# Kernel tuning notes

Hardware: AMD Instinct MI355X
Metric: run time of the kernel (lower is better)

The kernel has to match this reference:

```python
import jax, jax.numpy as jnp
import numpy as np

B, D = 65536, 365

def _linp(k, fan_in, fan_out):
    # torch nn.Linear default init: U(-1/sqrt(fan_in), 1/sqrt(fan_in))
    kw, kb = jax.random.split(k)
    bound = 1.0 / np.sqrt(fan_in)
    W = jax.random.uniform(kw, (fan_in, fan_out), jnp.float32, -bound, bound)
    b = jax.random.uniform(kb, (fan_out,), jnp.float32, -bound, bound)
    return W, b

def setup_inputs() -> dict:
    key = jax.random.key(0)
    ks = jax.random.split(key, 9)
    x = jax.random.normal(ks[0], (B, D), jnp.float32)
    W1, b1 = _linp(ks[1], D, 512)
    W2, b2 = _linp(ks[2], 512, 256)
    W3, b3 = _linp(ks[3], 256, 128)
    Ws, bs = _linp(ks[4], 6, 32)
    Wc1, bc1 = _linp(ks[5], 128 + 32, 64)
    Wc2, bc2 = _linp(ks[6], 64, 32)
    Wc3, bc3 = _linp(ks[7], 32, 1)
    return dict(x=x, W1=W1, b1=b1, W2=W2, b2=b2, W3=W3, b3=b3,
                Ws=Ws, bs=bs, Wc1=Wc1, bc1=bc1, Wc2=Wc2, bc2=bc2,
                Wc3=Wc3, bc3=bc3)

def _row_stats(x):
    # fused row-wise moments: mean, std (ddof=1), min, max, skew, kurtosis
    mu = jnp.mean(x, axis=1, keepdims=True)          # [B,1]
    c = x - mu                                        # [B,D]
    var1 = jnp.sum(c * c, axis=1) / (x.shape[1] - 1)  # unbiased, matches torch.std()
    sigma = jnp.sqrt(var1)
    m3 = jnp.mean(c ** 3, axis=1)
    m4 = jnp.mean(c ** 4, axis=1)
    skew = m3 / (sigma ** 3 + 1e-8)
    kurt = m4 / (sigma ** 4 + 1e-8)
    return jnp.stack([mu[:, 0], sigma, jnp.min(x, axis=1), jnp.max(x, axis=1), skew, kurt], axis=1)

def reference(x, W1, b1, W2, b2, W3, b3, Ws, bs, Wc1, bc1, Wc2, bc2, Wc3, bc3):
    h = jax.nn.relu(x @ W1 + b1)
    h = jax.nn.relu(h @ W2 + b2)
    seq = jax.nn.relu(h @ W3 + b3)            # [B,128]
    stat = _row_stats(x) @ Ws + bs            # [B,32]
    comb = jnp.concatenate([seq, stat], axis=1)
    c = jax.nn.relu(comb @ Wc1 + bc1)
    c = jax.nn.relu(c @ Wc2 + bc2)
    out = jax.nn.sigmoid(c @ Wc3 + bc3)       # [B,1]
    return out[:, 0]
```

## Files before the change

### kernel.cpp

```cpp
#include <hip/hip_runtime.h>
#include <math.h>

typedef __attribute__((ext_vector_type(8)))  short short8;
typedef __attribute__((ext_vector_type(16))) float float16;

#define DEVI __device__ __forceinline__

DEVI short f2bf(float f) {
    unsigned u = __float_as_uint(f);
    u = (u + 0x7fffu + ((u >> 16) & 1u)) >> 16;
    return (short)u;
}
DEVI unsigned pk2(float a, float b) {
    return (unsigned)(unsigned short)f2bf(a) | ((unsigned)(unsigned short)f2bf(b) << 16);
}
DEVI float16 mfma16(short8 a, short8 b, float16 c) {
    return __builtin_amdgcn_mfma_f32_32x32x16_bf16(a, b, c, 0, 0, 0);
}
DEVI int rowof(int r, int h) { return (r & 3) + 8 * (r >> 2) + 4 * h; }
DEVI short8 lds8(const short* p) { return *(const short8*)p; }
DEVI short8 gld8(const short* p) { return *(const short8*)p; }

#define W1T_OFF  0
#define W2T_OFF  188416
#define W3T_OFF  319488
#define WC1T_OFF 352256
#define WC2T_OFF 362496

__global__ void prep_v2(const float* __restrict__ W1, const float* __restrict__ W2,
                        const float* __restrict__ W3, const float* __restrict__ Wc1,
                        const float* __restrict__ Wc2, short* __restrict__ ws) {
    __shared__ short T[16 * 72];
    int b = blockIdx.x, t = threadIdx.x;
    const float* src; int K, N; size_t base; int kc, nb;
    if (b < 184)        {            src = W1;  K = 365; N = 512; base = W1T_OFF;  kc = b >> 3;  nb = b & 7; }
    else if (b < 312)   { int l = b - 184; src = W2;  K = 512; N = 256; base = W2T_OFF;  kc = l >> 2;  nb = l & 3; }
    else if (b < 344)   { int l = b - 312; src = W3;  K = 256; N = 128; base = W3T_OFF;  kc = l >> 1;  nb = l & 1; }
    else if (b < 354)   {            src = Wc1; K = 160; N = 64;  base = WC1T_OFF; kc = b - 344; nb = 0; }
    else                {            src = Wc2; K = 64;  N = 32;  base = WC2T_OFF; kc = b - 354; nb = 0; }
    int n = nb * 64 + (t & 63);
    int kr = t >> 6;
    #pragma unroll
    for (int i = 0; i < 4; ++i) {
        int krow = kr + 4 * i;
        int k = kc * 16 + krow;
        float v = (k < K && n < N) ? src[(size_t)k * N + n] : 0.f;
        T[krow * 72 + (t & 63)] = f2bf(v);
    }
    __syncthreads();
    int n2 = t >> 2, ksq = (t & 3) * 4;
    int ng = nb * 64 + n2;
    if (ng < N) {
        unsigned lo = (unsigned)(unsigned short)T[ksq * 72 + n2]
                    | ((unsigned)(unsigned short)T[(ksq + 1) * 72 + n2] << 16);
        unsigned hi = (unsigned)(unsigned short)T[(ksq + 2) * 72 + n2]
                    | ((unsigned)(unsigned short)T[(ksq + 3) * 72 + n2] << 16);
        uint2 d; d.x = lo; d.y = hi;
        *(uint2*)(ws + base + ((size_t)kc * N + ng) * 16 + ksq) = d;
    }
}

__global__ __launch_bounds__(512, 4)
void fused_v4(const float* __restrict__ x,
              const float* __restrict__ b1f, const float* __restrict__ b2f,
              const float* __restrict__ b3f, const float* __restrict__ Wsf,
              const float* __restrict__ bsf, const float* __restrict__ bc1f,
              const float* __restrict__ bc2f, const float* __restrict__ Wc3f,
              const float* __restrict__ bc3f,
              const short* __restrict__ wsw, float* __restrict__ out)
{
    __shared__ __align__(16) char smem[65536];
    short* XT    = (short*)smem;
    short* SB    = (short*)(smem + 48128);
    short* C1    = (short*)smem;
    short* FEATL = (short*)(smem + 12288);
    float* C2    = (float*)(smem + 20480);

    const short* W1t  = wsw + W1T_OFF;
    const short* W2t  = wsw + W2T_OFF;
    const short* W3t  = wsw + W3T_OFF;
    const short* Wc1t = wsw + WC1T_OFF;
    const short* Wc2t = wsw + WC2T_OFF;

    const int tid  = (int)threadIdx.x;
    const int lane = tid & 63;
    const int wv   = tid >> 6;
    const int m    = lane & 31;
    const int h    = lane >> 5;
    const int rowBase = (int)blockIdx.x * 64;

    float bb1a = b1f[32 * wv + m];
    float bb1b = b1f[256 + 32 * wv + m];
    float bb2  = b2f[32 * wv + m];
    float bb3  = b3f[32 * (wv & 3) + m];

    const int r0 = tid >> 3, j0 = tid & 7;
    const float* xrow = x + (size_t)(rowBase + r0) * 365;
    float s1 = 0.f, s2 = 0.f, s3 = 0.f, s4 = 0.f, mn = 1e30f, mx = -1e30f;
    #pragma unroll
    for (int i = 0; i < 6; ++i) {
        int o = j0 + 8 * i;
        if (o <= 45) {
            float xf[8];
            #pragma unroll
            for (int jj = 0; jj < 8; ++jj) {
                int col = o * 8 + jj;
                xf[jj] = (col < 365) ? xrow[col] : 0.f;
            }
            #pragma unroll
            for (int jj = 0; jj < 8; ++jj) {
                int col = o * 8 + jj;
                if (col < 365) {
                    float v = xf[jj], v2 = v * v;
                    s1 += v; s2 += v2; s3 += v2 * v; s4 += v2 * v2;
                    mn = fminf(mn, v); mx = fmaxf(mx, v);
                }
            }
            int4 w4;
            w4.x = (int)pk2(xf[0], xf[1]); w4.y = (int)pk2(xf[2], xf[3]);
            w4.z = (int)pk2(xf[4], xf[5]); w4.w = (int)pk2(xf[6], xf[7]);
            *(int4*)(XT + r0 * 376 + o * 8) = w4;
        }
    }
    #pragma unroll
    for (int off = 1; off <= 4; off <<= 1) {
        s1 += __shfl_xor(s1, off); s2 += __shfl_xor(s2, off);
        s3 += __shfl_xor(s3, off); s4 += __shfl_xor(s4, off);
        mn = fminf(mn, __shfl_xor(mn, off)); mx = fmaxf(mx, __shfl_xor(mx, off));
    }
    unsigned fdw0, fdw1;
    {
        float mean  = s1 * (1.0f / 365.0f);
        float var1  = (s2 - 365.0f * mean * mean) * (1.0f / 364.0f);
        float sigma = sqrtf(var1);
        float m3 = (s3 - 3.0f * mean * s2) * (1.0f / 365.0f) + 2.0f * mean * mean * mean;
        float mm = mean * mean;
        float m4 = (s4 - 4.0f * mean * s3 + 6.0f * mm * s2) * (1.0f / 365.0f) - 3.0f * mm * mm;
        float sg2 = sigma * sigma;
        float skew = m3 / (sigma * sg2 + 1e-8f);
        float kurt = m4 / (sg2 * sg2 + 1e-8f);
        float st[6] = { mean, sigma, mn, mx, skew, kurt };
        float f[4];
        #pragma unroll
        for (int c0 = 0; c0 < 4; ++c0) {
            int c = 4 * j0 + c0;
            float acc = bsf[c];
            #pragma unroll
            for (int jj = 0; jj < 6; ++jj) acc += st[jj] * Wsf[jj * 32 + c];
            f[c0] = acc;
        }
        fdw0 = pk2(f[0], f[1]); fdw1 = pk2(f[2], f[3]);
    }
    __syncthreads();

    float16 ha0, ha1;
    #pragma unroll
    for (int i = 0; i < 16; ++i) { ha0[i] = 0.f; ha1[i] = 0.f; }

    const short* Ap0  = XT + m * 376 + h * 8;
    const short* Ap1  = XT + (32 + m) * 376 + h * 8;
    const short* A2p0 = SB + m * 136 + h * 8;
    const short* A2p1 = SB + (32 + m) * 136 + h * 8;
    const int stcol = 32 * (wv & 3) + m;

    #pragma unroll
    for (int p = 0; p < 2; ++p) {
        float16 ga0, ga1;
        #pragma unroll
        for (int i = 0; i < 16; ++i) { ga0[i] = 0.f; ga1[i] = 0.f; }
        const short* B1 = W1t + (256 * p + 32 * wv + m) * 16 + h * 8;
        #pragma unroll
        for (int kc = 0; kc < 23; ++kc) {
            short8 b  = gld8(B1 + kc * 8192);
            short8 a0 = lds8(Ap0 + kc * 16);
            short8 a1 = lds8(Ap1 + kc * 16);
            ga0 = mfma16(a0, b, ga0);
            ga1 = mfma16(a1, b, ga1);
        }
        float bb = p ? bb1b : bb1a;
        #pragma unroll
        for (int s = 0; s < 2; ++s) {
            int sl = 2 * p + s;
            __syncthreads();
            if ((wv >> 2) == s) {
                #pragma unroll
                for (int r = 0; r < 16; ++r) {
                    SB[rowof(r, h) * 136 + stcol]        = f2bf(fmaxf(ga0[r] + bb, 0.f));
                    SB[(32 + rowof(r, h)) * 136 + stcol] = f2bf(fmaxf(ga1[r] + bb, 0.f));
                }
            }
            __syncthreads();
            const short* B2 = W2t + sl * 8 * 4096 + (32 * wv + m) * 16 + h * 8;
            #pragma unroll
            for (int i = 0; i < 8; ++i) {
                short8 b  = gld8(B2 + i * 4096);
                short8 a0 = lds8(A2p0 + i * 16);
                short8 a1 = lds8(A2p1 + i * 16);
                ha0 = mfma16(a0, b, ha0);
                ha1 = mfma16(a1, b, ha1);
            }
        }
    }

    float16 g3;
    #pragma unroll
    for (int i = 0; i < 16; ++i) g3[i] = 0.f;
    const short* A3p = SB + ((wv >> 2) * 32 + m) * 136 + h * 8;
    #pragma unroll
    for (int t = 0; t < 2; ++t) {
        __syncthreads();
        if ((wv >> 2) == t) {
            #pragma unroll
            for (int r = 0; r < 16; ++r) {
                SB[rowof(r, h) * 136 + stcol]        = f2bf(fmaxf(ha0[r] + bb2, 0.f));
                SB[(32 + rowof(r, h)) * 136 + stcol] = f2bf(fmaxf(ha1[r] + bb2, 0.f));
            }
        }
        __syncthreads();
        const short* B3 = W3t + t * 8 * 2048 + (32 * (wv & 3) + m) * 16 + h * 8;
        #pragma unroll
        for (int i = 0; i < 8; ++i) {
            short8 b = gld8(B3 + i * 2048);
            short8 a = lds8(A3p + i * 16);
            g3 = mfma16(a, b, g3);
        }
    }

    __syncthreads();
    {
        int rb = (wv >> 2) * 32;
        #pragma unroll
        for (int r = 0; r < 16; ++r)
            SB[(rb + rowof(r, h)) * 136 + stcol] = f2bf(fmaxf(g3[r] + bb3, 0.f));
        *(unsigned*)(FEATL + r0 * 40 + 4 * j0)     = fdw0;
        *(unsigned*)(FEATL + r0 * 40 + 4 * j0 + 2) = fdw1;
    }
    __syncthreads();

    if (wv < 4) {
        int m4 = wv & 1, c4 = wv >> 1;
        const short* B4 = Wc1t + (32 * c4 + m) * 16 + h * 8;
        const short* A4 = SB + (m4 * 32 + m) * 136 + h * 8;
        float16 g4;
        #pragma unroll
        for (int i = 0; i < 16; ++i) g4[i] = 0.f;
        #pragma unroll
        for (int i = 0; i < 8; ++i) {
            short8 b = gld8(B4 + i * 1024);
            short8 a = lds8(A4 + i * 16);
            g4 = mfma16(a, b, g4);
        }
        const short* AF = FEATL + (m4 * 32 + m) * 40 + h * 8;
        #pragma unroll
        for (int i = 0; i < 2; ++i) {
            short8 b = gld8(B4 + (8 + i) * 1024);
            short8 a = lds8(AF + i * 16);
            g4 = mfma16(a, b, g4);
        }
        float bb = bc1f[32 * c4 + m];
        #pragma unroll
        for (int r = 0; r < 16; ++r)
            C1[(m4 * 32 + rowof(r, h)) * 72 + 32 * c4 + m] = f2bf(fmaxf(g4[r] + bb, 0.f));
    }
    __syncthreads();

    if (wv < 2) {
        const short* B5 = Wc2t + m * 16 + h * 8;
        const short* A5 = C1 + (wv * 32 + m) * 72 + h * 8;
        float16 g5;
        #pragma unroll
        for (int i = 0; i < 16; ++i) g5[i] = 0.f;
        #pragma unroll
        for (int i = 0; i < 4; ++i) {
            short8 b = gld8(B5 + i * 512);
            short8 a = lds8(A5 + i * 16);
            g5 = mfma16(a, b, g5);
        }
        float bb = bc2f[m];
        #pragma unroll
        for (int r = 0; r < 16; ++r)
            C2[(wv * 32 + rowof(r, h)) * 33 + m] = fmaxf(g5[r] + bb, 0.f);
    }
    __syncthreads();

    if (tid < 64) {
        float z = bc3f[0];
        #pragma unroll
        for (int i = 0; i < 32; ++i) z += C2[tid * 33 + i] * Wc3f[i];
        out[rowBase + tid] = 1.0f / (1.0f + expf(-z));
    }
}

extern "C" void kernel_launch(void* const* d_in, const int* in_sizes, int n_in,
                              void* d_out, int out_size, void* d_ws, size_t ws_size,
                              hipStream_t stream)
{
    (void)in_sizes; (void)n_in; (void)out_size; (void)ws_size;
    const float* x   = (const float*)d_in[0];
    const float* W1  = (const float*)d_in[1];
    const float* b1  = (const float*)d_in[2];
    const float* W2  = (const float*)d_in[3];
    const float* b2  = (const float*)d_in[4];
    const float* W3  = (const float*)d_in[5];
    const float* b3  = (const float*)d_in[6];
    const float* Ws  = (const float*)d_in[7];
    const float* bs  = (const float*)d_in[8];
    const float* Wc1 = (const float*)d_in[9];
    const float* bc1 = (const float*)d_in[10];
    const float* Wc2 = (const float*)d_in[11];
    const float* bc2 = (const float*)d_in[12];
    const float* Wc3 = (const float*)d_in[13];
    const float* bc3 = (const float*)d_in[14];
    short* ws = (short*)d_ws;

    prep_v2<<<358, 256, 0, stream>>>(W1, W2, W3, Wc1, Wc2, ws);
    fused_v4<<<1024, 512, 0, stream>>>(x, b1, b2, b3, Ws, bs, bc1, bc2, Wc3, bc3,
                                       ws, (float*)d_out);
}
```

Before: 236.6 us.

## Halve block to 4 waves with 2x2 MFMA tiles and double-buffered LDS stages

The fused MLP kernel moves from 8 to 4 waves per 64-row block. Each wave now computes two column tiles by two row tiles, so every global weight fragment feeds twice as many MFMAs. Layer-1 outputs are held in registers as packed bf16 and written to two alternating LDS staging buffers, which removes many barriers. Register pressure rises a lot (four float16 accumulators plus the packed layer-1 array), and with fewer waves per CU there is less latency hiding.

```diff
diff --git a/kernel.cpp b/kernel.cpp
--- a/kernel.cpp
+++ b/kernel.cpp
@@ -60,8 +60,8 @@
     }
 }
 
-__global__ __launch_bounds__(512, 4)
-void fused_v4(const float* __restrict__ x,
+__global__ __launch_bounds__(256, 2)
+void fused_v5(const float* __restrict__ x,
               const float* __restrict__ b1f, const float* __restrict__ b2f,
               const float* __restrict__ b3f, const float* __restrict__ Wsf,
               const float* __restrict__ bsf, const float* __restrict__ bc1f,
@@ -69,12 +69,12 @@
               const float* __restrict__ bc3f,
               const short* __restrict__ wsw, float* __restrict__ out)
 {
-    __shared__ __align__(16) char smem[65536];
+    __shared__ __align__(16) char smem[53248];
     short* XT    = (short*)smem;
-    short* SB    = (short*)(smem + 48128);
-    short* C1    = (short*)smem;
-    short* FEATL = (short*)(smem + 12288);
-    float* C2    = (float*)(smem + 20480);
+    short* SB0   = (short*)smem;
+    short* SB1   = (short*)(smem + 17408);
+    float* C2f   = (float*)(smem + 36864);
+    short* FEATL = (short*)(smem + 48128);
 
     const short* W1t  = wsw + W1T_OFF;
     const short* W2t  = wsw + W2T_OFF;
@@ -89,17 +89,23 @@
     const int h    = lane >> 5;
     const int rowBase = (int)blockIdx.x * 64;
 
-    float bb1a = b1f[32 * wv + m];
-    float bb1b = b1f[256 + 32 * wv + m];
-    float bb2  = b2f[32 * wv + m];
-    float bb3  = b3f[32 * (wv & 3) + m];
-
-    const int r0 = tid >> 3, j0 = tid & 7;
+    float bb1[2][2], bb2[2];
+    #pragma unroll
+    for (int p = 0; p < 2; ++p)
+    #pragma unroll
+    for (int ct = 0; ct < 2; ++ct) bb1[p][ct] = b1f[256 * p + 64 * wv + 32 * ct + m];
+    bb2[0] = b2f[64 * wv + m]; bb2[1] = b2f[64 * wv + 32 + m];
+    float bb3  = b3f[32 * wv + m];
+    float bbc1 = bc1f[32 * (wv & 1) + m];
+    float bbc2 = bc2f[m];
+
+    const int r0 = tid >> 2, q = tid & 2 ? (tid & 3) : (tid & 3);
+    const int qq = tid & 3;
     const float* xrow = x + (size_t)(rowBase + r0) * 365;
     float s1 = 0.f, s2 = 0.f, s3 = 0.f, s4 = 0.f, mn = 1e30f, mx = -1e30f;
     #pragma unroll
-    for (int i = 0; i < 6; ++i) {
-        int o = j0 + 8 * i;
+    for (int i = 0; i < 12; ++i) {
+        int o = qq + 4 * i;
         if (o <= 45) {
             float xf[8];
             #pragma unroll
@@ -123,12 +129,11 @@
         }
     }
     #pragma unroll
-    for (int off = 1; off <= 4; off <<= 1) {
+    for (int off = 1; off <= 2; off <<= 1) {
         s1 += __shfl_xor(s1, off); s2 += __shfl_xor(s2, off);
         s3 += __shfl_xor(s3, off); s4 += __shfl_xor(s4, off);
         mn = fminf(mn, __shfl_xor(mn, off)); mx = fmaxf(mx, __shfl_xor(mx, off));
     }
-    unsigned fdw0, fdw1;
     {
         float mean  = s1 * (1.0f / 365.0f);
         float var1  = (s2 - 365.0f * mean * mean) * (1.0f / 364.0f);
@@ -140,153 +145,180 @@
         float skew = m3 / (sigma * sg2 + 1e-8f);
         float kurt = m4 / (sg2 * sg2 + 1e-8f);
         float st[6] = { mean, sigma, mn, mx, skew, kurt };
-        float f[4];
-        #pragma unroll
-        for (int c0 = 0; c0 < 4; ++c0) {
-            int c = 4 * j0 + c0;
+        float f[8];
+        #pragma unroll
+        for (int c0 = 0; c0 < 8; ++c0) {
+            int c = 8 * qq + c0;
             float acc = bsf[c];
             #pragma unroll
             for (int jj = 0; jj < 6; ++jj) acc += st[jj] * Wsf[jj * 32 + c];
             f[c0] = acc;
         }
-        fdw0 = pk2(f[0], f[1]); fdw1 = pk2(f[2], f[3]);
-    }
-    __syncthreads();
-
-    float16 ha0, ha1;
-    #pragma unroll
-    for (int i = 0; i < 16; ++i) { ha0[i] = 0.f; ha1[i] = 0.f; }
-
-    const short* Ap0  = XT + m * 376 + h * 8;
-    const short* Ap1  = XT + (32 + m) * 376 + h * 8;
-    const short* A2p0 = SB + m * 136 + h * 8;
-    const short* A2p1 = SB + (32 + m) * 136 + h * 8;
-    const int stcol = 32 * (wv & 3) + m;
-
+        int4 w4;
+        w4.x = (int)pk2(f[0], f[1]); w4.y = (int)pk2(f[2], f[3]);
+        w4.z = (int)pk2(f[4], f[5]); w4.w = (int)pk2(f[6], f[7]);
+        *(int4*)(FEATL + r0 * 40 + 8 * qq) = w4;
+    }
+    __syncthreads();
+
+    const short* Ap0 = XT + m * 376 + h * 8;
+    const short* Ap1 = Ap0 + 32 * 376;
+    unsigned park[2][2][2][8];
     #pragma unroll
     for (int p = 0; p < 2; ++p) {
-        float16 ga0, ga1;
-        #pragma unroll
-        for (int i = 0; i < 16; ++i) { ga0[i] = 0.f; ga1[i] = 0.f; }
-        const short* B1 = W1t + (256 * p + 32 * wv + m) * 16 + h * 8;
+        float16 c00, c01, c10, c11;
+        #pragma unroll
+        for (int i = 0; i < 16; ++i) { c00[i] = 0.f; c01[i] = 0.f; c10[i] = 0.f; c11[i] = 0.f; }
+        const short* B1 = W1t + (256 * p + 64 * wv + m) * 16 + h * 8;
         #pragma unroll
         for (int kc = 0; kc < 23; ++kc) {
-            short8 b  = gld8(B1 + kc * 8192);
+            short8 b0 = gld8(B1 + kc * 8192);
+            short8 b1 = gld8(B1 + 512 + kc * 8192);
             short8 a0 = lds8(Ap0 + kc * 16);
             short8 a1 = lds8(Ap1 + kc * 16);
-            ga0 = mfma16(a0, b, ga0);
-            ga1 = mfma16(a1, b, ga1);
-        }
-        float bb = p ? bb1b : bb1a;
-        #pragma unroll
-        for (int s = 0; s < 2; ++s) {
-            int sl = 2 * p + s;
-            __syncthreads();
-            if ((wv >> 2) == s) {
-                #pragma unroll
-                for (int r = 0; r < 16; ++r) {
-                    SB[rowof(r, h) * 136 + stcol]        = f2bf(fmaxf(ga0[r] + bb, 0.f));
-                    SB[(32 + rowof(r, h)) * 136 + stcol] = f2bf(fmaxf(ga1[r] + bb, 0.f));
-                }
+            c00 = mfma16(a0, b0, c00);
+            c01 = mfma16(a1, b0, c01);
+            c10 = mfma16(a0, b1, c10);
+            c11 = mfma16(a1, b1, c11);
+        }
+        #pragma unroll
+        for (int rr = 0; rr < 8; ++rr) {
+            park[p][0][0][rr] = pk2(fmaxf(c00[2*rr] + bb1[p][0], 0.f), fmaxf(c00[2*rr+1] + bb1[p][0], 0.f));
+            park[p][0][1][rr] = pk2(fmaxf(c01[2*rr] + bb1[p][0], 0.f), fmaxf(c01[2*rr+1] + bb1[p][0], 0.f));
+            park[p][1][0][rr] = pk2(fmaxf(c10[2*rr] + bb1[p][1], 0.f), fmaxf(c10[2*rr+1] + bb1[p][1], 0.f));
+            park[p][1][1][rr] = pk2(fmaxf(c11[2*rr] + bb1[p][1], 0.f), fmaxf(c11[2*rr+1] + bb1[p][1], 0.f));
+        }
+    }
+    __syncthreads();
+
+    float16 H00, H01, H10, H11;
+    #pragma unroll
+    for (int i = 0; i < 16; ++i) { H00[i] = 0.f; H01[i] = 0.f; H10[i] = 0.f; H11[i] = 0.f; }
+    const short* A2r0 = SB0 + m * 136 + h * 8;
+    #pragma unroll
+    for (int s = 0; s < 4; ++s) {
+        short* SBs = (s & 1) ? SB1 : SB0;
+        if ((wv >> 1) == (s & 1)) {
+            int p = s >> 1;
+            int cb = 64 * (wv & 1) + m;
+            #pragma unroll
+            for (int ct = 0; ct < 2; ++ct)
+            #pragma unroll
+            for (int rt = 0; rt < 2; ++rt)
+            #pragma unroll
+            for (int rr = 0; rr < 8; ++rr) {
+                unsigned pv = park[p][ct][rt][rr];
+                int row = rt * 32 + rowof(2 * rr, h);
+                SBs[row * 136 + cb + 32 * ct]       = (short)(pv & 0xffffu);
+                SBs[(row + 1) * 136 + cb + 32 * ct] = (short)(pv >> 16);
             }
-            __syncthreads();
-            const short* B2 = W2t + sl * 8 * 4096 + (32 * wv + m) * 16 + h * 8;
-            #pragma unroll
-            for (int i = 0; i < 8; ++i) {
-                short8 b  = gld8(B2 + i * 4096);
-                short8 a0 = lds8(A2p0 + i * 16);
-                short8 a1 = lds8(A2p1 + i * 16);
-                ha0 = mfma16(a0, b, ha0);
-                ha1 = mfma16(a1, b, ha1);
+        }
+        __syncthreads();
+        const short* A0p = SBs + m * 136 + h * 8;
+        const short* A1p = A0p + 32 * 136;
+        const short* B2 = W2t + (64 * wv + m) * 16 + h * 8 + s * 32768;
+        #pragma unroll
+        for (int i = 0; i < 8; ++i) {
+            short8 b0 = gld8(B2 + i * 4096);
+            short8 b1 = gld8(B2 + 512 + i * 4096);
+            short8 a0 = lds8(A0p + i * 16);
+            short8 a1 = lds8(A1p + i * 16);
+            H00 = mfma16(a0, b0, H00);
+            H01 = mfma16(a1, b0, H01);
+            H10 = mfma16(a0, b1, H10);
+            H11 = mfma16(a1, b1, H11);
+        }
+    }
+    (void)A2r0;
+
+    float16 S0, S1;
+    #pragma unroll
+    for (int i = 0; i < 16; ++i) { S0[i] = 0.f; S1[i] = 0.f; }
+    #pragma unroll
+    for (int t = 0; t < 2; ++t) {
+        short* SBs = t ? SB1 : SB0;
+        if ((wv >> 1) == t) {
+            int cb = 64 * (wv & 1) + m;
+            #pragma unroll
+            for (int rr = 0; rr < 8; ++rr) {
+                int rw0 = rowof(2 * rr, h);
+                SBs[rw0 * 136 + cb]              = f2bf(fmaxf(H00[2*rr]   + bb2[0], 0.f));
+                SBs[(rw0 + 1) * 136 + cb]        = f2bf(fmaxf(H00[2*rr+1] + bb2[0], 0.f));
+                SBs[(32 + rw0) * 136 + cb]       = f2bf(fmaxf(H01[2*rr]   + bb2[0], 0.f));
+                SBs[(33 + rw0) * 136 + cb]       = f2bf(fmaxf(H01[2*rr+1] + bb2[0], 0.f));
+                SBs[rw0 * 136 + cb + 32]         = f2bf(fmaxf(H10[2*rr]   + bb2[1], 0.f));
+                SBs[(rw0 + 1) * 136 + cb + 32]   = f2bf(fmaxf(H10[2*rr+1] + bb2[1], 0.f));
+                SBs[(32 + rw0) * 136 + cb + 32]  = f2bf(fmaxf(H11[2*rr]   + bb2[1], 0.f));
+                SBs[(33 + rw0) * 136 + cb + 32]  = f2bf(fmaxf(H11[2*rr+1] + bb2[1], 0.f));
             }
         }
-    }
-
-    float16 g3;
-    #pragma unroll
-    for (int i = 0; i < 16; ++i) g3[i] = 0.f;
-    const short* A3p = SB + ((wv >> 2) * 32 + m) * 136 + h * 8;
-    #pragma unroll
-    for (int t = 0; t < 2; ++t) {
         __syncthreads();
-        if ((wv >> 2) == t) {
-            #pragma unroll
-            for (int r = 0; r < 16; ++r) {
-                SB[rowof(r, h) * 136 + stcol]        = f2bf(fmaxf(ha0[r] + bb2, 0.f));
-                SB[(32 + rowof(r, h)) * 136 + stcol] = f2bf(fmaxf(ha1[r] + bb2, 0.f));
-            }
-        }
-        __syncthreads();
-        const short* B3 = W3t + t * 8 * 2048 + (32 * (wv & 3) + m) * 16 + h * 8;
+        const short* A0p = SBs + m * 136 + h * 8;
+        const short* A1p = A0p + 32 * 136;
+        const short* B3 = W3t + (32 * wv + m) * 16 + h * 8 + t * 16384;
         #pragma unroll
         for (int i = 0; i < 8; ++i) {
-            short8 b = gld8(B3 + i * 2048);
-            short8 a = lds8(A3p + i * 16);
-            g3 = mfma16(a, b, g3);
-        }
-    }
-
-    __syncthreads();
+            short8 b  = gld8(B3 + i * 2048);
+            short8 a0 = lds8(A0p + i * 16);
+            short8 a1 = lds8(A1p + i * 16);
+            S0 = mfma16(a0, b, S0);
+            S1 = mfma16(a1, b, S1);
+        }
+    }
+
     {
-        int rb = (wv >> 2) * 32;
+        int cb = 32 * wv + m;
+        #pragma unroll
+        for (int rr = 0; rr < 8; ++rr) {
+            int rw0 = rowof(2 * rr, h);
+            SB0[rw0 * 136 + cb]        = f2bf(fmaxf(S0[2*rr]   + bb3, 0.f));
+            SB0[(rw0 + 1) * 136 + cb]  = f2bf(fmaxf(S0[2*rr+1] + bb3, 0.f));
+            SB0[(32 + rw0) * 136 + cb] = f2bf(fmaxf(S1[2*rr]   + bb3, 0.f));
+            SB0[(33 + rw0) * 136 + cb] = f2bf(fmaxf(S1[2*rr+1] + bb3, 0.f));
+        }
+    }
+    __syncthreads();
+
+    {
+        int rt4 = wv >> 1, c4 = wv & 1;
+        float16 g4;
+        #pragma unroll
+        for (int i = 0; i < 16; ++i) g4[i] = 0.f;
+        const short* A4 = SB0 + (rt4 * 32 + m) * 136 + h * 8;
+        const short* B4 = Wc1t + (32 * c4 + m) * 16 + h * 8;
+        #pragma unroll
+        for (int i = 0; i < 8; ++i)
+            g4 = mfma16(lds8(A4 + i * 16), gld8(B4 + i * 1024), g4);
+        const short* AF = FEATL + (rt4 * 32 + m) * 40 + h * 8;
+        #pragma unroll
+        for (int i = 0; i < 2; ++i)
+            g4 = mfma16(lds8(AF + i * 16), gld8(B4 + (8 + i) * 1024), g4);
+        short* C1 = SB1;
         #pragma unroll
         for (int r = 0; r < 16; ++r)
-            SB[(rb + rowof(r, h)) * 136 + stcol] = f2bf(fmaxf(g3[r] + bb3, 0.f));
-        *(unsigned*)(FEATL + r0 * 40 + 4 * j0)     = fdw0;
-        *(unsigned*)(FEATL + r0 * 40 + 4 * j0 + 2) = fdw1;
-    }
-    __syncthreads();
-
-    if (wv < 4) {
-        int m4 = wv & 1, c4 = wv >> 1;
-        const short* B4 = Wc1t + (32 * c4 + m) * 16 + h * 8;
-        const short* A4 = SB + (m4 * 32 + m) * 136 + h * 8;
-        float16 g4;
-        #pragma unroll
-        for (int i = 0; i < 16; ++i) g4[i] = 0.f;
-        #pragma unroll
-        for (int i = 0; i < 8; ++i) {
-            short8 b = gld8(B4 + i * 1024);
-            short8 a = lds8(A4 + i * 16);
-            g4 = mfma16(a, b, g4);
-        }
-        const short* AF = FEATL + (m4 * 32 + m) * 40 + h * 8;
-        #pragma unroll
-        for (int i = 0; i < 2; ++i) {
-            short8 b = gld8(B4 + (8 + i) * 1024);
-            short8 a = lds8(AF + i * 16);
-            g4 = mfma16(a, b, g4);
-        }
-        float bb = bc1f[32 * c4 + m];
+            C1[(rt4 * 32 + rowof(r, h)) * 72 + 32 * c4 + m] = f2bf(fmaxf(g4[r] + bbc1, 0.f));
+    }
+    __syncthreads();
+
+    if (wv < 2) {
+        const short* A5 = SB1 + (32 * wv + m) * 72 + h * 8;
+        const short* B5 = Wc2t + m * 16 + h * 8;
+        float16 g5;
+        #pragma unroll
+        for (int i = 0; i < 16; ++i) g5[i] = 0.f;
+        #pragma unroll
+        for (int i = 0; i < 4; ++i)
+            g5 = mfma16(lds8(A5 + i * 16), gld8(B5 + i * 512), g5);
         #pragma unroll
         for (int r = 0; r < 16; ++r)
-            C1[(m4 * 32 + rowof(r, h)) * 72 + 32 * c4 + m] = f2bf(fmaxf(g4[r] + bb, 0.f));
-    }
-    __syncthreads();
-
-    if (wv < 2) {
-        const short* B5 = Wc2t + m * 16 + h * 8;
-        const short* A5 = C1 + (wv * 32 + m) * 72 + h * 8;
-        float16 g5;
-        #pragma unroll
-        for (int i = 0; i < 16; ++i) g5[i] = 0.f;
-        #pragma unroll
-        for (int i = 0; i < 4; ++i) {
-            short8 b = gld8(B5 + i * 512);
-            short8 a = lds8(A5 + i * 16);
-            g5 = mfma16(a, b, g5);
-        }
-        float bb = bc2f[m];
-        #pragma unroll
-        for (int r = 0; r < 16; ++r)
-            C2[(wv * 32 + rowof(r, h)) * 33 + m] = fmaxf(g5[r] + bb, 0.f);
+            C2f[(32 * wv + rowof(r, h)) * 33 + m] = fmaxf(g5[r] + bbc2, 0.f);
     }
     __syncthreads();
 
     if (tid < 64) {
         float z = bc3f[0];
         #pragma unroll
-        for (int i = 0; i < 32; ++i) z += C2[tid * 33 + i] * Wc3f[i];
+        for (int i = 0; i < 32; ++i) z += C2f[tid * 33 + i] * Wc3f[i];
         out[rowBase + tid] = 1.0f / (1.0f + expf(-z));
     }
 }
@@ -314,6 +346,6 @@
     short* ws = (short*)d_ws;
 
     prep_v2<<<358, 256, 0, stream>>>(W1, W2, W3, Wc1, Wc2, ws);
-    fused_v4<<<1024, 512, 0, stream>>>(x, b1, b2, b3, Ws, bs, bc1, bc2, Wc3, bc3,
+    fused_v5<<<1024, 256, 0, stream>>>(x, b1, b2, b3, Ws, bs, bc1, bc2, Wc3, bc3,
                                        ws, (float*)d_out);
 }
```

Measured after the change: 245.5 us. 3.8% more time.
